# Kernel optimization log

Hardware: AMD Instinct MI355X
Metric: run time of the kernel (lower is better)

Reference implementation:

```python
import jax, jax.numpy as jnp
import numpy as np

ALPHA = 0.25
GAMMA = 2.0
W_CLASS = W_BBOX = W_GIOU = W_MASK = W_DICE = W_PROJ = 1.0
EPS = 1e-8


def box_cxcywh_to_xyxy(b):
    cx, cy, w, h = jnp.split(b, 4, axis=-1)
    return jnp.concatenate([cx - 0.5 * w, cy - 0.5 * h, cx + 0.5 * w, cy + 0.5 * h], axis=-1)


def dice_coef(inputs, targets):
    # inputs: logits [N, D]; targets: binary [M, D]
    s = jax.nn.sigmoid(inputs)
    num = 2.0 * jnp.einsum('nd,md->nm', s, targets)
    den = s.sum(-1)[:, None] + targets.sum(-1)[None, :]
    return (num + 1.0) / (den + 1.0)  # [N, M]


def sigmoid_focal_coef(inputs, targets):
    # inputs: logits [N, D]; targets: binary [M, D] -> [N, M]
    x = inputs[:, None, :]
    t = targets[None, :, :]
    p = jax.nn.sigmoid(x)
    # BCE-with-logits, numerically stable
    ce = jnp.maximum(x, 0.0) - x * t + jnp.log1p(jnp.exp(-jnp.abs(x)))
    p_t = p * t + (1.0 - p) * (1.0 - t)
    alpha_t = ALPHA * t + (1.0 - ALPHA) * (1.0 - t)
    return (alpha_t * ce * (1.0 - p_t) ** GAMMA).mean(-1)


def giou_cost(src_xyxy, tgt_xyxy):
    # src [nf, nq, 4], tgt [nf, 1, 4] -> cost [nf, nq, 1]
    a1 = (src_xyxy[..., 2] - src_xyxy[..., 0]) * (src_xyxy[..., 3] - src_xyxy[..., 1])
    a2 = (tgt_xyxy[..., 2] - tgt_xyxy[..., 0]) * (tgt_xyxy[..., 3] - tgt_xyxy[..., 1])
    lt = jnp.maximum(src_xyxy[:, :, None, :2], tgt_xyxy[:, None, :, :2])
    rb = jnp.minimum(src_xyxy[:, :, None, 2:], tgt_xyxy[:, None, :, 2:])
    wh = jnp.clip(rb - lt, 0.0)
    inter = wh[..., 0] * wh[..., 1]
    union = a1[:, :, None] + a2[:, None, :] - inter
    iou = inter / union
    ltc = jnp.minimum(src_xyxy[:, :, None, :2], tgt_xyxy[:, None, :, :2])
    rbc = jnp.maximum(src_xyxy[:, :, None, 2:], tgt_xyxy[:, None, :, 2:])
    whc = jnp.clip(rbc - ltc, 0.0)
    areac = whc[..., 0] * whc[..., 1]
    giou = iou - (areac - union) / areac
    return -giou


def cost_matrix_one(logits, boxes, masks, tmask, tbox, tvalid):
    # logits [nf,nq,1], boxes [nf,nq,4], masks [nf,nq,H,W], tmask [nf,H,W], tbox [nf,4], tvalid [nf]
    p = jax.nn.sigmoid(logits[..., 0])  # [nf, nq]
    neg = (1.0 - ALPHA) * p ** GAMMA * (-jnp.log(1.0 - p + EPS))
    pos = ALPHA * (1.0 - p) ** GAMMA * (-jnp.log(p + EPS))
    w = (tvalid != 0).astype(p.dtype)  # valid-frame mask replaces python `continue`
    cost_class = (((pos - neg) * w[:, None]).sum(0) / w.sum())[:, None]  # [nq, 1]

    cost_bbox = jnp.abs(boxes[:, :, None, :] - tbox[:, None, None, :]).sum(-1).mean(0)  # [nq, 1]
    cost_giou = giou_cost(box_cxcywh_to_xyxy(boxes), box_cxcywh_to_xyxy(tbox[:, None, :])).mean(0)

    out_mask = jnp.transpose(masks, (1, 0, 2, 3))  # [nq, nf, H, W]
    nq = out_mask.shape[0]
    flat_src = out_mask.reshape(nq, -1)
    flat_tgt = tmask.reshape(1, -1)
    cost_mask = sigmoid_focal_coef(flat_src, flat_tgt)  # [nq, 1]
    cost_dice = -dice_coef(flat_src, flat_tgt)

    src_y = jnp.max(out_mask, axis=2, keepdims=True).reshape(nq, -1)  # [nq, nf*W]
    src_x = jnp.max(out_mask, axis=3, keepdims=True).reshape(nq, -1)  # [nq, nf*H]
    tgt_y = jnp.max(tmask[None], axis=2, keepdims=True).reshape(1, -1)
    tgt_x = jnp.max(tmask[None], axis=3, keepdims=True).reshape(1, -1)
    cost_proj = -0.5 * (dice_coef(src_y, tgt_y) + dice_coef(src_x, tgt_x))

    C = (W_CLASS * cost_class + W_BBOX * cost_bbox + W_GIOU * cost_giou
         + W_MASK * cost_mask + W_DICE * cost_dice + W_PROJ * cost_proj)
    return C  # [nq, 1]


def setup_inputs() -> dict:
    key = jax.random.key(0)
    k = jax.random.split(key, 6)
    bs, nf, nq, H, W = 2, 8, 300, 96, 96
    pred_logits = jax.random.normal(k[0], (bs, nf, nq, 1), dtype=jnp.float32)
    pred_boxes = jax.random.uniform(k[1], (bs, nf, nq, 4), dtype=jnp.float32)
    pred_masks = jax.random.normal(k[2], (bs, nf, nq, H, W), dtype=jnp.float32)
    target_masks = (jax.random.uniform(k[3], (bs, nf, H, W)) < 0.3).astype(jnp.float32)
    tgt_boxes = jax.random.uniform(k[4], (bs, nf, 4), dtype=jnp.float32)
    tgt_valid = jnp.ones((bs, nf), dtype=jnp.int32)
    valid_pad = jnp.zeros((bs, H, W), dtype=bool)
    return {"pred_logits": pred_logits, "pred_boxes": pred_boxes, "pred_masks": pred_masks,
            "target_masks": target_masks, "tgt_boxes": tgt_boxes, "tgt_valid": tgt_valid,
            "valid_pad": valid_pad}


def reference(pred_logits, pred_boxes, pred_masks, target_masks, tgt_boxes, tgt_valid, valid_pad):
    # zero out predictions over padded regions (masked_fill with valid[:, None, None])
    masks = jnp.where(valid_pad[:, None, None, :, :], 0.0, pred_masks)
    C = jax.vmap(cost_matrix_one)(pred_logits, pred_boxes, masks, target_masks, tgt_boxes, tgt_valid)
    src_ind = jnp.argmin(C, axis=1).astype(jnp.int64)  # [bs, 1]
    tgt_ind = jnp.zeros_like(src_ind)
    return C, src_ind, tgt_ind
```

## Files before the change

kernel.cpp:

```cpp
#include <hip/hip_runtime.h>
#include <math.h>

#define NF 8
#define NQ 300
#define HSZ 96
#define WSZ 96
#define HW (HSZ*WSZ)
#define DTOT (NF*HW)
#define NBF 16

#define WS_TGTY  0
#define WS_TGTX  1536
#define WS_TSUM  3072
#define WS_YSUM  3088
#define WS_XSUM  3104
#define WS_TBITS 3136
#define WS_PBITS 7744
#define WS_PART  8320

__device__ __forceinline__ float sigmoid_fast(float x) {
    float e = __expf(-fabsf(x));
    float inv = __builtin_amdgcn_rcpf(1.f + e);
    return x >= 0.f ? inv : e * inv;
}

#define NTT 1024
__global__ __launch_bounds__(NTT)
void targets_kernel(const float* __restrict__ tm, const unsigned char* __restrict__ vpad,
                    float* __restrict__ ws) {
    int bf = blockIdx.x, t = threadIdx.x;
    int lane = t & 63, wid = t >> 6;
    __shared__ float tile[HSZ * 97];
    __shared__ float redt[16 * 3];
    const float* base = tm + (size_t)bf * HW;
    unsigned* tbw = (unsigned*)(ws + WS_TBITS) + bf * 288;

    float tsum = 0.f;
    #pragma unroll
    for (int it = 0; it < 9; ++it) {
        int e = it * NTT + t;
        float v = base[e];
        tsum += v;
        tile[e + e / 96] = v;
        unsigned long long m = __ballot(v != 0.f);
        int word = it * 32 + wid * 2;
        if (lane == 0)       tbw[word]     = (unsigned)m;
        else if (lane == 32) tbw[word + 1] = (unsigned)(m >> 32);
    }
    if ((bf & 7) == 0) {
        const unsigned char* vb = vpad + (size_t)(bf >> 3) * HW;
        unsigned* pbw = (unsigned*)(ws + WS_PBITS) + (bf >> 3) * 288;
        #pragma unroll
        for (int it = 0; it < 9; ++it) {
            int e = it * NTT + t;
            unsigned long long m = __ballot(vb[e] != 0);
            int word = it * 32 + wid * 2;
            if (lane == 0)       pbw[word]     = (unsigned)m;
            else if (lane == 32) pbw[word + 1] = (unsigned)(m >> 32);
        }
    }
    __syncthreads();

    float ysum = 0.f, xsum = 0.f;
    if (t < 96) {
        float m = -INFINITY;
        #pragma unroll 8
        for (int h = 0; h < HSZ; ++h) m = fmaxf(m, tile[h * 97 + t]);
        ws[WS_TGTY + bf * 96 + t] = m;
        ysum = m;
    } else if (t < 192) {
        int hh = t - 96;
        float m = -INFINITY;
        #pragma unroll 8
        for (int w = 0; w < WSZ; ++w) m = fmaxf(m, tile[hh * 97 + w]);
        ws[WS_TGTX + bf * 96 + hh] = m;
        xsum = m;
    }
    float s0 = tsum, s1 = ysum, s2 = xsum;
    #pragma unroll
    for (int off = 32; off > 0; off >>= 1) {
        s0 += __shfl_down(s0, off, 64);
        s1 += __shfl_down(s1, off, 64);
        s2 += __shfl_down(s2, off, 64);
    }
    if (lane == 0) { redt[wid * 3] = s0; redt[wid * 3 + 1] = s1; redt[wid * 3 + 2] = s2; }
    __syncthreads();
    if (t == 0) {
        float a0 = 0.f, a1 = 0.f, a2 = 0.f;
        #pragma unroll
        for (int w = 0; w < 16; ++w) {
            a0 += redt[w * 3]; a1 += redt[w * 3 + 1]; a2 += redt[w * 3 + 2];
        }
        ws[WS_TSUM + bf] = a0;
        ws[WS_YSUM + bf] = a1;
        ws[WS_XSUM + bf] = a2;
    }
}

#define NTP 384
__global__ __launch_bounds__(NTP, 6)
void partial_kernel(const float* __restrict__ masks, const float* __restrict__ ws,
                    float* __restrict__ part) {
    int bid = blockIdx.x;
    int bf = bid / NQ;
    int q  = bid - bf * NQ;
    int b  = bf >> 3, f = bf & 7;
    int t  = threadIdx.x;
    int w4 = t % 24;
    int r0 = t / 24;
    int wsh = (t & 7) * 4;

    __shared__ float rp[96 * 25];
    __shared__ float cp[16 * 100];
    __shared__ float red[6][8];

    const float4* mrow = (const float4*)(masks + (size_t)bid * HW);
    const unsigned* tbw = (const unsigned*)(ws + WS_TBITS) + bf * 288;
    const unsigned* pbw = (const unsigned*)(ws + WS_PBITS) + b * 288;

    float4 xv[6];
    unsigned tw[6], pw[6];
    #pragma unroll
    for (int k = 0; k < 6; ++k) xv[k] = mrow[k * NTP + t];
    #pragma unroll
    for (int k = 0; k < 6; ++k) tw[k] = tbw[k * 48 + (t >> 3)];
    #pragma unroll
    for (int k = 0; k < 6; ++k) pw[k] = pbw[k * 48 + (t >> 3)];

    float focal = 0.f, dnum = 0.f, dden = 0.f;
    float cm0 = -INFINITY, cm1 = -INFINITY, cm2 = -INFINITY, cm3 = -INFINITY;

    #pragma unroll
    for (int k = 0; k < 6; ++k) {
        unsigned tn = (tw[k] >> wsh) & 0xFu;
        unsigned pn = (pw[k] >> wsh) & 0xFu;
        float xs[4] = {xv[k].x, xv[k].y, xv[k].z, xv[k].w};
        if (pn) {
            #pragma unroll
            for (int j = 0; j < 4; ++j) if ((pn >> j) & 1u) xs[j] = 0.f;
        }
        float rmx = -INFINITY;
        #pragma unroll
        for (int j = 0; j < 4; ++j) {
            float x = xs[j];
            float tg = (float)((tn >> j) & 1u);
            float e2 = __expf(x);
            float se = 1.f + e2;
            float inv = __builtin_amdgcn_rcpf(se);
            float s = e2 * inv;
            float L = __logf(se);
            float ce = fmaf(-x, tg, L);
            float omp = fmaf(tg, fmaf(-2.f, s, 1.f), s);
            float at = fmaf(tg, -0.5f, 0.75f);
            focal = fmaf(at * ce, omp * omp, focal);
            dnum = fmaf(s, tg, dnum);
            dden += s;
            rmx = fmaxf(rmx, x);
        }
        cm0 = fmaxf(cm0, xs[0]); cm1 = fmaxf(cm1, xs[1]);
        cm2 = fmaxf(cm2, xs[2]); cm3 = fmaxf(cm3, xs[3]);
        rp[(16 * k + r0) * 25 + w4] = rmx;
    }
    {
        float4 cmv = {cm0, cm1, cm2, cm3};
        *(float4*)&cp[r0 * 100 + w4 * 4] = cmv;
    }
    __syncthreads();

    float v0 = focal, v1 = dnum, v2 = dden, v3 = 0.f, v4 = 0.f, v5 = 0.f, v6 = 0.f;
    if (t < 96) {
        float m = -INFINITY;
        #pragma unroll
        for (int p = 0; p < 16; ++p) m = fmaxf(m, cp[p * 100 + t]);
        float sg = sigmoid_fast(m);
        v4 = sg;
        v3 = sg * ws[WS_TGTY + bf * 96 + t];
    } else if (t < 192) {
        int r = t - 96;
        float m = rp[r * 25];
        #pragma unroll
        for (int c = 1; c < 24; ++c) m = fmaxf(m, rp[r * 25 + c]);
        float sg = sigmoid_fast(m);
        v6 = sg;
        v5 = sg * ws[WS_TGTX + bf * 96 + r];
    }
    #pragma unroll
    for (int off = 32; off > 0; off >>= 1) {
        v0 += __shfl_down(v0, off, 64);
        v1 += __shfl_down(v1, off, 64);
        v2 += __shfl_down(v2, off, 64);
        v3 += __shfl_down(v3, off, 64);
        v4 += __shfl_down(v4, off, 64);
        v5 += __shfl_down(v5, off, 64);
        v6 += __shfl_down(v6, off, 64);
    }
    int wid = t >> 6, lane = t & 63;
    if (lane == 0) {
        red[wid][0] = v0; red[wid][1] = v1; red[wid][2] = v2; red[wid][3] = v3;
        red[wid][4] = v4; red[wid][5] = v5; red[wid][6] = v6;
    }
    __syncthreads();
    if (t == 0) {
        float* o = part + (size_t)((b * NQ + q) * NF + f) * 8;
        #pragma unroll
        for (int i = 0; i < 7; ++i)
            o[i] = red[0][i] + red[1][i] + red[2][i] + red[3][i] + red[4][i] + red[5][i];
    }
}

#define NTF 640
__global__ __launch_bounds__(NTF)
void combine_argmin_kernel(const float* __restrict__ logits, const float* __restrict__ boxes,
                           const float* __restrict__ tbox, const int* __restrict__ tvalid,
                           const float* __restrict__ ws, float* __restrict__ out,
                           int write_idx) {
    int t = threadIdx.x;
    __shared__ float sv[2 * NQ];

    if (t < 2 * NQ) {
        int b = t / NQ, q = t - b * NQ;

        const float* pbase = ws + WS_PART + (size_t)t * (NF * 8);
        float focal = 0.f, dnum = 0.f, dden = 0.f;
        float pYn = 0.f, pYd = 0.f, pXn = 0.f, pXd = 0.f;
        float tsum = 0.f, ysum = 0.f, xsum = 0.f;
        #pragma unroll
        for (int f = 0; f < NF; ++f) {
            int bf = b * NF + f;
            const float* p = pbase + f * 8;
            focal += p[0]; dnum += p[1]; dden += p[2];
            pYn += p[3]; pYd += p[4]; pXn += p[5]; pXd += p[6];
            tsum += ws[WS_TSUM + bf];
            ysum += ws[WS_YSUM + bf];
            xsum += ws[WS_XSUM + bf];
        }
        float cost_mask = focal / (float)DTOT;
        float cost_dice = -(2.f * dnum + 1.f) / (dden + tsum + 1.f);
        float coefY = (2.f * pYn + 1.f) / (pYd + ysum + 1.f);
        float coefX = (2.f * pXn + 1.f) / (pXd + xsum + 1.f);
        float cost_proj = -0.5f * (coefY + coefX);

        float wsum = 0.f, cls = 0.f, cb = 0.f, cg = 0.f;
        #pragma unroll
        for (int f = 0; f < NF; ++f) {
            float wv = (tvalid[b * NF + f] != 0) ? 1.f : 0.f;
            wsum += wv;
            float lg = logits[(b * NF + f) * NQ + q];
            float p = sigmoid_fast(lg);
            float negc = 0.75f * p * p * (-__logf(1.f - p + 1e-8f));
            float posc = 0.25f * (1.f - p) * (1.f - p) * (-__logf(p + 1e-8f));
            cls += (posc - negc) * wv;

            const float* bx = boxes + (size_t)((b * NF + f) * NQ + q) * 4;
            const float* tb = tbox + (b * NF + f) * 4;
            float cx = bx[0], cy = bx[1], bw = bx[2], bh = bx[3];
            float tcx = tb[0], tcy = tb[1], tbw = tb[2], tbh = tb[3];
            cb += fabsf(cx - tcx) + fabsf(cy - tcy) + fabsf(bw - tbw) + fabsf(bh - tbh);
            float sx1 = cx - 0.5f * bw, sy1 = cy - 0.5f * bh;
            float sx2 = cx + 0.5f * bw, sy2 = cy + 0.5f * bh;
            float tx1 = tcx - 0.5f * tbw, ty1 = tcy - 0.5f * tbh;
            float tx2 = tcx + 0.5f * tbw, ty2 = tcy + 0.5f * tbh;
            float a1 = (sx2 - sx1) * (sy2 - sy1), a2 = (tx2 - tx1) * (ty2 - ty1);
            float iw = fmaxf(fminf(sx2, tx2) - fmaxf(sx1, tx1), 0.f);
            float ih = fmaxf(fminf(sy2, ty2) - fmaxf(sy1, ty1), 0.f);
            float inter = iw * ih;
            float uni = a1 + a2 - inter;
            float iou = inter / uni;
            float cw = fmaxf(fmaxf(sx2, tx2) - fminf(sx1, tx1), 0.f);
            float chh = fmaxf(fmaxf(sy2, ty2) - fminf(sy1, ty1), 0.f);
            float areac = cw * chh;
            cg += -(iou - (areac - uni) / areac);
        }
        cls /= wsum;
        cb *= 0.125f;
        cg *= 0.125f;
        float val = cls + cb + cg + cost_mask + cost_dice + cost_proj;
        out[t] = val;
        sv[t] = val;
    }
    __syncthreads();

    int wid = t >> 6, lane = t & 63;
    if (wid < 2 && write_idx) {
        int b = wid;
        float best = INFINITY;
        int bi = 0x7fffffff;
        for (int q = lane; q < NQ; q += 64) {
            float v = sv[b * NQ + q];
            if (v < best) { best = v; bi = q; }
        }
        #pragma unroll
        for (int off = 32; off > 0; off >>= 1) {
            float ov = __shfl_down(best, off, 64);
            int oi = __shfl_down(bi, off, 64);
            if (ov < best || (ov == best && oi < bi)) { best = ov; bi = oi; }
        }
        if (lane == 0) {
            out[2 * NQ + b] = (float)bi;
            out[2 * NQ + 2 + b] = 0.f;
        }
    }
}

extern "C" void kernel_launch(void* const* d_in, const int* in_sizes, int n_in,
                              void* d_out, int out_size, void* d_ws, size_t ws_size,
                              hipStream_t stream) {
    const float* logits = (const float*)d_in[0];
    const float* boxes  = (const float*)d_in[1];
    const float* masks  = (const float*)d_in[2];
    const float* tmask  = (const float*)d_in[3];
    const float* tbox   = (const float*)d_in[4];
    const int*   tvalid = (const int*)d_in[5];
    const unsigned char* vpad = (const unsigned char*)d_in[6];
    float* out = (float*)d_out;
    float* ws  = (float*)d_ws;

    targets_kernel<<<NBF, NTT, 0, stream>>>(tmask, vpad, ws);
    partial_kernel<<<NBF * NQ, NTP, 0, stream>>>(masks, ws, ws + WS_PART);
    int write_idx = (out_size >= 2 * NQ + 4) ? 1 : 0;
    combine_argmin_kernel<<<1, NTF, 0, stream>>>(logits, boxes, tbox, tvalid, ws, out,
                                                 write_idx);
}
```

Before: 291.0 us.

## Process three query planes per block with software-pipelined inline-asm loads

```diff
diff --git a/kernel.cpp b/kernel.cpp
--- a/kernel.cpp
+++ b/kernel.cpp
@@ -18,11 +18,24 @@
 #define WS_PBITS 7744
 #define WS_PART  8320
 
+typedef float f32x4 __attribute__((ext_vector_type(4)));
+
 __device__ __forceinline__ float sigmoid_fast(float x) {
     float e = __expf(-fabsf(x));
     float inv = __builtin_amdgcn_rcpf(1.f + e);
     return x >= 0.f ? inv : e * inv;
 }
+
+__device__ __forceinline__ f32x4 gload4(const f32x4* p) {
+    f32x4 d;
+    asm volatile("global_load_dwordx4 %0, %1, off" : "=v"(d) : "v"(p));
+    return d;
+}
+
+#define WAITV(N) do { \
+    asm volatile("s_waitcnt vmcnt(" #N ")" ::: "memory"); \
+    __builtin_amdgcn_sched_barrier(0); \
+} while (0)
 
 #define NTT 1024
 __global__ __launch_bounds__(NTT)
@@ -98,114 +111,157 @@
 }
 
 #define NTP 384
-__global__ __launch_bounds__(NTP, 6)
+#define QPB 3
+#define NPLB (NQ/QPB)
+
+#define EL(X, TB) do { \
+    float x_ = (X); float tg_ = (float)(TB); \
+    float e2_ = __expf(x_); \
+    float se_ = 1.f + e2_; \
+    float inv_ = __builtin_amdgcn_rcpf(se_); \
+    float s_ = e2_ * inv_; \
+    float L_ = __logf(se_); \
+    float ce_ = fmaf(-x_, tg_, L_); \
+    float omp_ = fmaf(tg_, fmaf(-2.f, s_, 1.f), s_); \
+    float at_ = fmaf(tg_, -0.5f, 0.75f); \
+    focal = fmaf(at_ * ce_, omp_ * omp_, focal); \
+    dnum = fmaf(s_, tg_, dnum); \
+    dden += s_; \
+    rmx = fmaxf(rmx, x_); \
+} while (0)
+
+#define KSTEP(KK, XV) do { \
+    unsigned tn_ = (tw[KK] >> wsh) & 0xFu; \
+    unsigned pn_ = (pw[KK] >> wsh) & 0xFu; \
+    float xs0 = (XV).x, xs1 = (XV).y, xs2 = (XV).z, xs3 = (XV).w; \
+    if (pn_) { \
+        if (pn_ & 1u) xs0 = 0.f; \
+        if (pn_ & 2u) xs1 = 0.f; \
+        if (pn_ & 4u) xs2 = 0.f; \
+        if (pn_ & 8u) xs3 = 0.f; \
+    } \
+    float rmx = -INFINITY; \
+    EL(xs0, tn_ & 1u); EL(xs1, (tn_ >> 1) & 1u); \
+    EL(xs2, (tn_ >> 2) & 1u); EL(xs3, (tn_ >> 3) & 1u); \
+    cm0 = fmaxf(cm0, xs0); cm1 = fmaxf(cm1, xs1); \
+    cm2 = fmaxf(cm2, xs2); cm3 = fmaxf(cm3, xs3); \
+    rp[(16 * (KK) + r0) * 25 + w4] = rmx; \
+} while (0)
+
+#define PLANE(X0,X1,X2,X3,X4,X5, QI) do { \
+    float focal = 0.f, dnum = 0.f, dden = 0.f; \
+    float cm0 = -INFINITY, cm1 = -INFINITY, cm2 = -INFINITY, cm3 = -INFINITY; \
+    KSTEP(0, X0); KSTEP(1, X1); KSTEP(2, X2); \
+    KSTEP(3, X3); KSTEP(4, X4); KSTEP(5, X5); \
+    { f32x4 cmv_ = {cm0, cm1, cm2, cm3}; *(f32x4*)&cp[r0 * 100 + w4 * 4] = cmv_; } \
+    asm volatile("s_waitcnt lgkmcnt(0)" ::: "memory"); \
+    __builtin_amdgcn_s_barrier(); \
+    __builtin_amdgcn_sched_barrier(0); \
+    float v0 = focal, v1 = dnum, v2 = dden, v3 = 0.f, v4 = 0.f, v5 = 0.f, v6 = 0.f; \
+    if (t < 96) { \
+        float m_ = -INFINITY; \
+        _Pragma("unroll") \
+        for (int p_ = 0; p_ < 16; ++p_) m_ = fmaxf(m_, cp[p_ * 100 + t]); \
+        float sg_ = sigmoid_fast(m_); \
+        v4 = sg_; v3 = sg_ * gy; \
+    } else if (t < 192) { \
+        int r_ = t - 96; \
+        float m_ = rp[r_ * 25]; \
+        _Pragma("unroll") \
+        for (int c_ = 1; c_ < 24; ++c_) m_ = fmaxf(m_, rp[r_ * 25 + c_]); \
+        float sg_ = sigmoid_fast(m_); \
+        v6 = sg_; v5 = sg_ * gx; \
+    } \
+    _Pragma("unroll") \
+    for (int off_ = 32; off_ > 0; off_ >>= 1) { \
+        v0 += __shfl_down(v0, off_, 64); \
+        v1 += __shfl_down(v1, off_, 64); \
+        v2 += __shfl_down(v2, off_, 64); \
+        v3 += __shfl_down(v3, off_, 64); \
+        v4 += __shfl_down(v4, off_, 64); \
+        v5 += __shfl_down(v5, off_, 64); \
+        v6 += __shfl_down(v6, off_, 64); \
+    } \
+    if ((t & 63) == 0) { \
+        int wid_ = t >> 6; \
+        red[wid_][0] = v0; red[wid_][1] = v1; red[wid_][2] = v2; red[wid_][3] = v3; \
+        red[wid_][4] = v4; red[wid_][5] = v5; red[wid_][6] = v6; \
+    } \
+    asm volatile("s_waitcnt lgkmcnt(0)" ::: "memory"); \
+    __builtin_amdgcn_s_barrier(); \
+    __builtin_amdgcn_sched_barrier(0); \
+    if (t < 7) { \
+        float tot_ = red[0][t] + red[1][t] + red[2][t] + red[3][t] + red[4][t] + red[5][t]; \
+        part[(size_t)((b * NQ + (QI)) * NF + f) * 8 + t] = tot_; \
+    } \
+} while (0)
+
+__global__ __launch_bounds__(NTP, 4)
 void partial_kernel(const float* __restrict__ masks, const float* __restrict__ ws,
                     float* __restrict__ part) {
     int bid = blockIdx.x;
-    int bf = bid / NQ;
-    int q  = bid - bf * NQ;
-    int b  = bf >> 3, f = bf & 7;
-    int t  = threadIdx.x;
-    int w4 = t % 24;
-    int r0 = t / 24;
+    int bf  = bid / NPLB;
+    int q0  = (bid - bf * NPLB) * QPB;
+    int b   = bf >> 3, f = bf & 7;
+    int t   = threadIdx.x;
+    int w4  = t % 24;
+    int r0  = t / 24;
     int wsh = (t & 7) * 4;
 
     __shared__ float rp[96 * 25];
     __shared__ float cp[16 * 100];
     __shared__ float red[6][8];
 
-    const float4* mrow = (const float4*)(masks + (size_t)bid * HW);
     const unsigned* tbw = (const unsigned*)(ws + WS_TBITS) + bf * 288;
     const unsigned* pbw = (const unsigned*)(ws + WS_PBITS) + b * 288;
 
-    float4 xv[6];
     unsigned tw[6], pw[6];
     #pragma unroll
-    for (int k = 0; k < 6; ++k) xv[k] = mrow[k * NTP + t];
-    #pragma unroll
     for (int k = 0; k < 6; ++k) tw[k] = tbw[k * 48 + (t >> 3)];
     #pragma unroll
     for (int k = 0; k < 6; ++k) pw[k] = pbw[k * 48 + (t >> 3)];
-
-    float focal = 0.f, dnum = 0.f, dden = 0.f;
-    float cm0 = -INFINITY, cm1 = -INFINITY, cm2 = -INFINITY, cm3 = -INFINITY;
+    float gy = 0.f, gx = 0.f;
+    if (t < 96)       gy = ws[WS_TGTY + bf * 96 + t];
+    else if (t < 192) gx = ws[WS_TGTX + bf * 96 + (t - 96)];
 
     #pragma unroll
     for (int k = 0; k < 6; ++k) {
-        unsigned tn = (tw[k] >> wsh) & 0xFu;
-        unsigned pn = (pw[k] >> wsh) & 0xFu;
-        float xs[4] = {xv[k].x, xv[k].y, xv[k].z, xv[k].w};
-        if (pn) {
-            #pragma unroll
-            for (int j = 0; j < 4; ++j) if ((pn >> j) & 1u) xs[j] = 0.f;
-        }
-        float rmx = -INFINITY;
-        #pragma unroll
-        for (int j = 0; j < 4; ++j) {
-            float x = xs[j];
-            float tg = (float)((tn >> j) & 1u);
-            float e2 = __expf(x);
-            float se = 1.f + e2;
-            float inv = __builtin_amdgcn_rcpf(se);
-            float s = e2 * inv;
-            float L = __logf(se);
-            float ce = fmaf(-x, tg, L);
-            float omp = fmaf(tg, fmaf(-2.f, s, 1.f), s);
-            float at = fmaf(tg, -0.5f, 0.75f);
-            focal = fmaf(at * ce, omp * omp, focal);
-            dnum = fmaf(s, tg, dnum);
-            dden += s;
-            rmx = fmaxf(rmx, x);
-        }
-        cm0 = fmaxf(cm0, xs[0]); cm1 = fmaxf(cm1, xs[1]);
-        cm2 = fmaxf(cm2, xs[2]); cm3 = fmaxf(cm3, xs[3]);
-        rp[(16 * k + r0) * 25 + w4] = rmx;
-    }
-    {
-        float4 cmv = {cm0, cm1, cm2, cm3};
-        *(float4*)&cp[r0 * 100 + w4 * 4] = cmv;
-    }
-    __syncthreads();
-
-    float v0 = focal, v1 = dnum, v2 = dden, v3 = 0.f, v4 = 0.f, v5 = 0.f, v6 = 0.f;
-    if (t < 96) {
-        float m = -INFINITY;
-        #pragma unroll
-        for (int p = 0; p < 16; ++p) m = fmaxf(m, cp[p * 100 + t]);
-        float sg = sigmoid_fast(m);
-        v4 = sg;
-        v3 = sg * ws[WS_TGTY + bf * 96 + t];
-    } else if (t < 192) {
-        int r = t - 96;
-        float m = rp[r * 25];
-        #pragma unroll
-        for (int c = 1; c < 24; ++c) m = fmaxf(m, rp[r * 25 + c]);
-        float sg = sigmoid_fast(m);
-        v6 = sg;
-        v5 = sg * ws[WS_TGTX + bf * 96 + r];
-    }
-    #pragma unroll
-    for (int off = 32; off > 0; off >>= 1) {
-        v0 += __shfl_down(v0, off, 64);
-        v1 += __shfl_down(v1, off, 64);
-        v2 += __shfl_down(v2, off, 64);
-        v3 += __shfl_down(v3, off, 64);
-        v4 += __shfl_down(v4, off, 64);
-        v5 += __shfl_down(v5, off, 64);
-        v6 += __shfl_down(v6, off, 64);
-    }
-    int wid = t >> 6, lane = t & 63;
-    if (lane == 0) {
-        red[wid][0] = v0; red[wid][1] = v1; red[wid][2] = v2; red[wid][3] = v3;
-        red[wid][4] = v4; red[wid][5] = v5; red[wid][6] = v6;
-    }
-    __syncthreads();
-    if (t == 0) {
-        float* o = part + (size_t)((b * NQ + q) * NF + f) * 8;
-        #pragma unroll
-        for (int i = 0; i < 7; ++i)
-            o[i] = red[0][i] + red[1][i] + red[2][i] + red[3][i] + red[4][i] + red[5][i];
-    }
+        asm volatile("" : "+v"(tw[k]));
+        asm volatile("" : "+v"(pw[k]));
+    }
+    asm volatile("" : "+v"(gy), "+v"(gx));
+
+    const f32x4* base = (const f32x4*)(masks + (size_t)(bf * NQ + q0) * HW);
+
+    f32x4 a0, a1, a2, a3, a4, a5, b0, b1, b2, b3, b4, b5;
+    a0 = gload4(base + 0 * NTP + t);
+    a1 = gload4(base + 1 * NTP + t);
+    a2 = gload4(base + 2 * NTP + t);
+    a3 = gload4(base + 3 * NTP + t);
+    a4 = gload4(base + 4 * NTP + t);
+    a5 = gload4(base + 5 * NTP + t);
+    b0 = gload4(base + 2304 + 0 * NTP + t);
+    b1 = gload4(base + 2304 + 1 * NTP + t);
+    b2 = gload4(base + 2304 + 2 * NTP + t);
+    b3 = gload4(base + 2304 + 3 * NTP + t);
+    b4 = gload4(base + 2304 + 4 * NTP + t);
+    b5 = gload4(base + 2304 + 5 * NTP + t);
+
+    WAITV(6);
+    PLANE(a0, a1, a2, a3, a4, a5, q0);
+
+    a0 = gload4(base + 4608 + 0 * NTP + t);
+    a1 = gload4(base + 4608 + 1 * NTP + t);
+    a2 = gload4(base + 4608 + 2 * NTP + t);
+    a3 = gload4(base + 4608 + 3 * NTP + t);
+    a4 = gload4(base + 4608 + 4 * NTP + t);
+    a5 = gload4(base + 4608 + 5 * NTP + t);
+
+    WAITV(6);
+    PLANE(b0, b1, b2, b3, b4, b5, q0 + 1);
+
+    WAITV(0);
+    PLANE(a0, a1, a2, a3, a4, a5, q0 + 2);
 }
 
 #define NTF 640
@@ -316,7 +372,7 @@
     float* ws  = (float*)d_ws;
 
     targets_kernel<<<NBF, NTT, 0, stream>>>(tmask, vpad, ws);
-    partial_kernel<<<NBF * NQ, NTP, 0, stream>>>(masks, ws, ws + WS_PART);
+    partial_kernel<<<NBF * NPLB, NTP, 0, stream>>>(masks, ws, ws + WS_PART);
     int write_idx = (out_size >= 2 * NQ + 4) ? 1 : 0;
     combine_argmin_kernel<<<1, NTF, 0, stream>>>(logits, boxes, tbox, tvalid, ws, out,
                                                  write_idx);
```

After: 336.1 us. +15.5%, slower.
